# Optimization experiments

Measured on AMD Instinct MI355X. Metric: run time of the kernel, lower is better.

The kernel has to match this reference:

```python
import jax, jax.numpy as jnp
import numpy as np

CH = 512
NUM_HEADS = 8
NUM_GROUPS = 32  # min(32, channels)
EPS = 1e-5


def setup_inputs() -> dict:
    key = jax.random.key(0)
    ks = jax.random.split(key, 4)
    B, C, H, W = 8, CH, 32, 32
    x = jax.random.normal(ks[0], (B, C, H, W), dtype=jnp.float32)
    gn_weight = jnp.ones((C,), dtype=jnp.float32)
    gn_bias = jnp.zeros((C,), dtype=jnp.float32)
    # 1x1 conv weights stored as [out_ch, in_ch] (kernel dims squeezed)
    qkv_weight = jax.random.normal(ks[1], (3 * C, C), dtype=jnp.float32) * (C ** -0.5)
    qkv_bias = jnp.zeros((3 * C,), dtype=jnp.float32)
    proj_weight = jax.random.normal(ks[2], (C, C), dtype=jnp.float32) * (C ** -0.5)
    proj_bias = jnp.zeros((C,), dtype=jnp.float32)
    return {
        "x": x,
        "gn_weight": gn_weight,
        "gn_bias": gn_bias,
        "qkv_weight": qkv_weight,
        "qkv_bias": qkv_bias,
        "proj_weight": proj_weight,
        "proj_bias": proj_bias,
    }


def _group_norm(x, weight, bias):
    B, C, H, W = x.shape
    g = x.reshape(B, NUM_GROUPS, C // NUM_GROUPS, H, W)
    mean = jnp.mean(g, axis=(2, 3, 4), keepdims=True)
    var = jnp.var(g, axis=(2, 3, 4), keepdims=True)
    g = (g - mean) * jax.lax.rsqrt(var + EPS)
    g = g.reshape(B, C, H, W)
    return g * weight[None, :, None, None] + bias[None, :, None, None]


def reference(x, gn_weight, gn_bias, qkv_weight, qkv_bias, proj_weight, proj_bias):
    B, C, H, W = x.shape
    nh = NUM_HEADS
    hc = C // nh
    N = H * W

    h = _group_norm(x, gn_weight, gn_bias)
    # 1x1 conv == per-pixel matmul
    qkv = jnp.einsum('oc,bchw->bohw', qkv_weight, h) + qkv_bias[None, :, None, None]
    q, k, v = jnp.split(qkv, 3, axis=1)
    # b (h c) x y -> b h c (x y)
    q = q.reshape(B, nh, hc, N)
    k = k.reshape(B, nh, hc, N)
    v = v.reshape(B, nh, hc, N)

    scale = hc ** -0.5
    attn = jnp.einsum('bhci,bhcj->bhij', q, k) * scale  # [B, nh, N, N]
    attn = jax.nn.softmax(attn, axis=-1)
    out = jnp.einsum('bhij,bhcj->bhci', attn, v)  # [B, nh, hc, N]
    out = out.reshape(B, C, H, W)
    out = jnp.einsum('oc,bchw->bohw', proj_weight, out) + proj_bias[None, :, None, None]
    return x + out
```

## Files before the change

kernel.cpp:

```cpp
#include <hip/hip_runtime.h>
#include <math.h>

#define B_   8
#define C_   512
#define N_   1024
#define NH_  8
#define HC_  64

typedef __attribute__((ext_vector_type(8))) short bf16x8;
typedef __attribute__((ext_vector_type(4))) float f32x4;

#define MFMA16(a, b, c) __builtin_amdgcn_mfma_f32_16x16x32_bf16(a, b, c, 0, 0, 0)

__device__ __forceinline__ unsigned short f2bf(float f) {
  unsigned u = __builtin_bit_cast(unsigned, f);
  u += 0x7fffu + ((u >> 16) & 1u);
  return (unsigned short)(u >> 16);
}

__device__ __forceinline__ unsigned short f2bf_trunc(float f) {
  return (unsigned short)(__builtin_bit_cast(unsigned, f) >> 16);
}

__device__ __forceinline__ unsigned pack2(float a, float b) {
  return (unsigned)f2bf(a) | ((unsigned)f2bf(b) << 16);
}

__device__ __forceinline__ void gll16(const void* g, void* l) {
  __builtin_amdgcn_global_load_lds(
      (const __attribute__((address_space(1))) unsigned int*)g,
      (__attribute__((address_space(3))) unsigned int*)l, 16, 0, 0);
}

__global__ __launch_bounds__(256) void prep(const float* __restrict__ x,
                                            const float* __restrict__ gw,
                                            const float* __restrict__ gb,
                                            const float* __restrict__ qkvw,
                                            const float* __restrict__ pw,
                                            unsigned short* __restrict__ hT,
                                            unsigned short* __restrict__ qkvw_bf,
                                            unsigned short* __restrict__ projw_bf) {
  const int t = threadIdx.x;
  if (blockIdx.x >= 256) {
    const int widx = blockIdx.x - 256;
    const float* src = (widx < 768) ? qkvw : pw;
    unsigned short* dst = (widx < 768) ? qkvw_bf : projw_bf;
    const int i = ((widx < 768) ? widx : widx - 768) * 1024 + t * 4;
    const float4 v = *(const float4*)(src + i);
    ushort4 o;
    o.x = f2bf(v.x); o.y = f2bf(v.y); o.z = f2bf(v.z); o.w = f2bf(v.w);
    *(ushort4*)(dst + i) = o;
    return;
  }
  const int b = blockIdx.x >> 5;
  const int g = blockIdx.x & 31;
  const float* xg = x + ((size_t)b * C_ + (size_t)g * 16) * N_;

  float4 xv[16];
  float s = 0.f, ss = 0.f;
#pragma unroll
  for (int k = 0; k < 16; ++k) {
    xv[k] = *(const float4*)(xg + (size_t)k * N_ + t * 4);
    s  += xv[k].x + xv[k].y + xv[k].z + xv[k].w;
    ss += xv[k].x * xv[k].x + xv[k].y * xv[k].y + xv[k].z * xv[k].z + xv[k].w * xv[k].w;
  }
#pragma unroll
  for (int off = 32; off > 0; off >>= 1) {
    s  += __shfl_down(s, off);
    ss += __shfl_down(ss, off);
  }
  __shared__ float rs[4], rss[4], sh_mi[2];
  if ((t & 63) == 0) { rs[t >> 6] = s; rss[t >> 6] = ss; }
  __syncthreads();
  if (t == 0) {
    s  = rs[0] + rs[1] + rs[2] + rs[3];
    ss = rss[0] + rss[1] + rss[2] + rss[3];
    const float mean = s * (1.f / 16384.f);
    const float var  = ss * (1.f / 16384.f) - mean * mean;
    sh_mi[0] = mean;
    sh_mi[1] = rsqrtf(var + 1e-5f);
  }
  __syncthreads();
  const float mean = sh_mi[0], inv = sh_mi[1];

  float sc[16], of[16];
#pragma unroll
  for (int k = 0; k < 16; ++k) {
    const int c = g * 16 + k;
    sc[k] = inv * gw[c];
    of[k] = gb[c] - mean * sc[k];
  }
#pragma unroll
  for (int r = 0; r < 4; ++r) {
    const int p = t * 4 + r;
    unsigned short* dst = hT + ((size_t)b * N_ + p) * C_ + g * 16;
    uint4 o0, o1;
#pragma unroll
    for (int k2 = 0; k2 < 4; ++k2) {
      const float a0 = ((const float*)&xv[k2 * 2 + 0])[r] * sc[k2 * 2 + 0] + of[k2 * 2 + 0];
      const float a1 = ((const float*)&xv[k2 * 2 + 1])[r] * sc[k2 * 2 + 1] + of[k2 * 2 + 1];
      ((unsigned*)&o0)[k2] = pack2(a0, a1);
      const float b0 = ((const float*)&xv[8 + k2 * 2 + 0])[r] * sc[8 + k2 * 2 + 0] + of[8 + k2 * 2 + 0];
      const float b1 = ((const float*)&xv[8 + k2 * 2 + 1])[r] * sc[8 + k2 * 2 + 1] + of[8 + k2 * 2 + 1];
      ((unsigned*)&o1)[k2] = pack2(b0, b1);
    }
    *(uint4*)(dst)     = o0;
    *(uint4*)(dst + 8) = o1;
  }
}

__global__ __launch_bounds__(256, 3) void gemm_qkv(
    const unsigned short* __restrict__ A, const float* __restrict__ bias,
    const unsigned short* __restrict__ BT, unsigned short* __restrict__ qkTout,
    unsigned short* __restrict__ vout) {
  __shared__ __attribute__((aligned(16))) short lds[128 * 136];
  const int t = threadIdx.x;
  const int lane = t & 63, w = t >> 6;
  const int lm = lane & 15, q = lane >> 4;
  const int wm = w >> 1, wn = w & 1;
  const int b = blockIdx.z;
  const int m0 = blockIdx.y * 128, n0 = blockIdx.x * 128;
  const unsigned short* Bb = BT + (size_t)b * N_ * C_;

  f32x4 acc[4][4];
#pragma unroll
  for (int i = 0; i < 4; ++i)
#pragma unroll
    for (int j = 0; j < 4; ++j) acc[i][j] = (f32x4){0.f, 0.f, 0.f, 0.f};

#define QKV_STAGE(k0, base_)                                                   \
  {                                                                            \
    _Pragma("unroll") for (int rr = 0; rr < 2; ++rr) {                         \
      const int rg = w * 2 + rr;                                               \
      gll16(A  + (size_t)(m0 + rg * 16 + lm) * C_ + (k0) + q * 8,              \
            (base_) + rg * 512);                                               \
      gll16(Bb + (size_t)(n0 + rg * 16 + lm) * C_ + (k0) + q * 8,              \
            (base_) + (8 + rg) * 512);                                         \
    }                                                                          \
  }

#define QKV_COMPUTE(base_)                                                     \
  {                                                                            \
    bf16x8 af[4];                                                              \
    _Pragma("unroll") for (int mi = 0; mi < 4; ++mi)                           \
      af[mi] = *(const bf16x8*)((base_) + (wm * 4 + mi) * 512 + lane * 8);     \
    _Pragma("unroll") for (int ni = 0; ni < 4; ++ni) {                         \
      const bf16x8 bfr =                                                       \
          *(const bf16x8*)((base_) + (8 + wn * 4 + ni) * 512 + lane * 8);      \
      _Pragma("unroll") for (int mi = 0; mi < 4; ++mi)                         \
        acc[mi][ni] = MFMA16(af[mi], bfr, acc[mi][ni]);                        \
    }                                                                          \
  }

  QKV_STAGE(0, lds)
  for (int it = 0; it < 15; ++it) {
    __syncthreads();
    short* nxt = lds + ((it + 1) & 1) * 8192;
    QKV_STAGE((it + 1) * 32, nxt)
    const short* cur = lds + (it & 1) * 8192;
    QKV_COMPUTE(cur)
  }
  __syncthreads();
  QKV_COMPUTE(lds + 8192)
#undef QKV_STAGE
#undef QKV_COMPUTE

  __syncthreads();
  if (blockIdx.y < 8) {
    const float qs = (blockIdx.y < 4) ? 0.18033688011112042f : 1.0f;
#pragma unroll
    for (int mi = 0; mi < 4; ++mi) {
#pragma unroll
      for (int ni = 0; ni < 4; ++ni) {
        const int pl = wn * 64 + ni * 16 + lm;
        const int ol0 = wm * 64 + mi * 16 + q * 4;
        ushort4 o4;
        o4.x = f2bf((acc[mi][ni][0] + bias[m0 + ol0 + 0]) * qs);
        o4.y = f2bf((acc[mi][ni][1] + bias[m0 + ol0 + 1]) * qs);
        o4.z = f2bf((acc[mi][ni][2] + bias[m0 + ol0 + 2]) * qs);
        o4.w = f2bf((acc[mi][ni][3] + bias[m0 + ol0 + 3]) * qs);
        *(ushort4*)&lds[pl * 136 + ol0] = o4;
      }
    }
    __syncthreads();
#pragma unroll
    for (int u = 0; u < 8; ++u) {
      const int flat = u * 256 + t;
      const int oc = flat & 15, pl = flat >> 4;
      *(uint4*)&qkTout[((size_t)b * N_ + n0 + pl) * 1024 + m0 + oc * 8] =
          *(const uint4*)&lds[pl * 136 + oc * 8];
    }
  } else {
#pragma unroll
    for (int mi = 0; mi < 4; ++mi)
#pragma unroll
      for (int ni = 0; ni < 4; ++ni) {
        const int pl = wn * 64 + ni * 16 + lm;
#pragma unroll
        for (int r = 0; r < 4; ++r) {
          const int ol = wm * 64 + mi * 16 + q * 4 + r;
          lds[ol * 136 + pl] = f2bf(acc[mi][ni][r] + bias[m0 + ol]);
        }
      }
    __syncthreads();
    const int c0 = m0 - 1024;
#pragma unroll
    for (int u = 0; u < 8; ++u) {
      const int flat = u * 256 + t;
      const int pc = flat & 15, ol = flat >> 4;
      *(uint4*)&vout[((size_t)b * 512 + c0 + ol) * N_ + n0 + pc * 8] =
          *(const uint4*)&lds[ol * 136 + pc * 8];
    }
  }
}

__global__ __launch_bounds__(256, 4) void gemm_proj(
    const unsigned short* __restrict__ A, const float* __restrict__ bias,
    const unsigned short* __restrict__ BT, const float* __restrict__ resid,
    float* __restrict__ outf) {
  __shared__ __attribute__((aligned(16))) short lds[32 * 512];
  const int t = threadIdx.x;
  const int lane = t & 63, w = t >> 6;
  const int lm = lane & 15, q = lane >> 4;
  const int wm = w >> 1, wn = w & 1;
  const int b = blockIdx.z;
  const int m0 = blockIdx.y * 64, n0 = blockIdx.x * 64;
  const unsigned short* Bb = BT + (size_t)b * N_ * C_;

  f32x4 acc[2][2];
#pragma unroll
  for (int i = 0; i < 2; ++i)
#pragma unroll
    for (int j = 0; j < 2; ++j) acc[i][j] = (f32x4){0.f, 0.f, 0.f, 0.f};

  for (int k0 = 0; k0 < C_; k0 += 128) {
    __syncthreads();
#pragma unroll
    for (int ks = 0; ks < 4; ++ks) {
      gll16(A  + (size_t)(m0 + w * 16 + lm) * C_ + k0 + ks * 32 + q * 8,
            lds + (w * 4 + ks) * 512);
      gll16(Bb + (size_t)(n0 + w * 16 + lm) * C_ + k0 + ks * 32 + q * 8,
            lds + (16 + w * 4 + ks) * 512);
    }
    __syncthreads();
#pragma unroll
    for (int ks = 0; ks < 4; ++ks) {
      bf16x8 af[2];
#pragma unroll
      for (int mi = 0; mi < 2; ++mi)
        af[mi] = *(const bf16x8*)(lds + ((wm * 2 + mi) * 4 + ks) * 512 + lane * 8);
#pragma unroll
      for (int ni = 0; ni < 2; ++ni) {
        const bf16x8 bfr =
            *(const bf16x8*)(lds + (16 + (wn * 2 + ni) * 4 + ks) * 512 + lane * 8);
#pragma unroll
        for (int mi = 0; mi < 2; ++mi)
          acc[mi][ni] = MFMA16(af[mi], bfr, acc[mi][ni]);
      }
    }
  }

#pragma unroll
  for (int mi = 0; mi < 2; ++mi)
#pragma unroll
    for (int ni = 0; ni < 2; ++ni) {
      const int col = n0 + wn * 32 + ni * 16 + lm;
#pragma unroll
      for (int r = 0; r < 4; ++r) {
        const int row = m0 + wm * 32 + mi * 16 + q * 4 + r;
        const size_t oi = ((size_t)b * 512 + row) * N_ + col;
        outf[oi] = acc[mi][ni][r] + bias[row] + resid[oi];
      }
    }
}

__global__ __launch_bounds__(256, 6) void attn_mfma(
    const unsigned short* __restrict__ qkT, const unsigned short* __restrict__ vbuf,
    unsigned short* __restrict__ aoT) {
  __shared__ __attribute__((aligned(16))) short lds[12800];
  short* Ks = lds;
  short* Vs = lds + 8 * 512;
  short* Pb = lds + 16 * 512;

  const int t = threadIdx.x;
  const int lane = t & 63, w = t >> 6;
  const int lm = lane & 15, q = lane >> 4;
  const int id = blockIdx.x;
  const int xcd = id & 7, slot = id >> 3;
  const int pair = xcd * 8 + (slot >> 4);
  const int b = pair >> 3, hh = pair & 7;
  const int i0 = (slot & 15) * 64;

  const unsigned short* QT = qkT + (size_t)b * N_ * 1024;
  const unsigned short* Vp = vbuf + ((size_t)b * 512 + hh * 64) * N_;
  short* Pw = Pb + w * 1152;

  bf16x8 af[2];
#pragma unroll
  for (int ks = 0; ks < 2; ++ks)
    af[ks] = *(const bf16x8*)(QT + (size_t)(i0 + w * 16 + lm) * 1024 +
                              hh * 64 + ks * 32 + q * 8);

  f32x4 accO[4], lrun = (f32x4){0.f, 0.f, 0.f, 0.f};
#pragma unroll
  for (int nc = 0; nc < 4; ++nc) accO[nc] = (f32x4){0.f, 0.f, 0.f, 0.f};

  for (int jt = 0; jt < 16; ++jt) {
    const int j0 = jt * 64;
    __syncthreads();
#pragma unroll
    for (int ks = 0; ks < 2; ++ks) {
      gll16(QT + (size_t)(j0 + w * 16 + lm) * 1024 + 512 + hh * 64 + ks * 32 + q * 8,
            Ks + (w * 2 + ks) * 512);
      gll16(Vp + (size_t)(w * 16 + lm) * N_ + j0 + ks * 32 + q * 8,
            Vs + (w * 2 + ks) * 512);
    }
    __syncthreads();

    f32x4 accS[4];
#pragma unroll
    for (int nj = 0; nj < 4; ++nj) accS[nj] = (f32x4){0.f, 0.f, 0.f, 0.f};
    __builtin_amdgcn_s_setprio(1);
#pragma unroll
    for (int nj = 0; nj < 4; ++nj)
#pragma unroll
      for (int ks = 0; ks < 2; ++ks) {
        const bf16x8 bfr = *(const bf16x8*)(Ks + (nj * 2 + ks) * 512 + lane * 8);
        accS[nj] = MFMA16(af[ks], bfr, accS[nj]);
      }
    __builtin_amdgcn_s_setprio(0);

#pragma unroll
    for (int nj = 0; nj < 4; ++nj)
#pragma unroll
      for (int r = 0; r < 4; ++r) {
        const float p = __builtin_exp2f(accS[nj][r]);
        accS[nj][r] = p;
        lrun[r] += p;
      }
#pragma unroll
    for (int nj = 0; nj < 4; ++nj)
#pragma unroll
      for (int r = 0; r < 4; ++r)
        Pw[(q * 4 + r) * 72 + nj * 16 + lm] = (short)f2bf_trunc(accS[nj][r]);

    __builtin_amdgcn_s_setprio(1);
#pragma unroll
    for (int ks = 0; ks < 2; ++ks) {
      const bf16x8 pf = *(const bf16x8*)(Pw + lm * 72 + ks * 32 + q * 8);
#pragma unroll
      for (int nc = 0; nc < 4; ++nc) {
        const bf16x8 vf = *(const bf16x8*)(Vs + (nc * 2 + ks) * 512 + lane * 8);
        accO[nc] = MFMA16(pf, vf, accO[nc]);
      }
    }
    __builtin_amdgcn_s_setprio(0);
  }

#pragma unroll
  for (int d = 1; d <= 8; d <<= 1)
#pragma unroll
    for (int r = 0; r < 4; ++r) lrun[r] += __shfl_xor(lrun[r], d);
  f32x4 linv;
#pragma unroll
  for (int r = 0; r < 4; ++r) linv[r] = 1.f / lrun[r];

#pragma unroll
  for (int nc = 0; nc < 4; ++nc)
#pragma unroll
    for (int r = 0; r < 4; ++r)
      Pw[(q * 4 + r) * 72 + nc * 16 + lm] = f2bf(accO[nc][r] * linv[r]);
  unsigned short* aob = aoT + (size_t)b * N_ * C_;
#pragma unroll
  for (int u = 0; u < 2; ++u) {
    const int flat = u * 64 + lane;
    const int c8 = flat & 7, i = flat >> 3;
    *(uint4*)&aob[(size_t)(i0 + w * 16 + i) * C_ + hh * 64 + c8 * 8] =
        *(const uint4*)&Pw[i * 72 + c8 * 8];
  }
}

extern "C" void kernel_launch(void* const* d_in, const int* in_sizes, int n_in,
                              void* d_out, int out_size, void* d_ws, size_t ws_size,
                              hipStream_t stream) {
  const float* x    = (const float*)d_in[0];
  const float* gw   = (const float*)d_in[1];
  const float* gb   = (const float*)d_in[2];
  const float* qkvw = (const float*)d_in[3];
  const float* qkvb = (const float*)d_in[4];
  const float* pw   = (const float*)d_in[5];
  const float* pb   = (const float*)d_in[6];
  float* out = (float*)d_out;

  unsigned short* hT       = (unsigned short*)d_ws;
  unsigned short* qkvw_bf  = hT + (size_t)B_ * N_ * C_;
  unsigned short* projw_bf = qkvw_bf + 1536 * 512;
  unsigned short* qkT      = projw_bf + 512 * 512;
  unsigned short* vbuf     = qkT + (size_t)B_ * N_ * 1024;
  unsigned short* aoTp     = vbuf + (size_t)B_ * 512 * N_;

  prep<<<1280, 256, 0, stream>>>(x, gw, gb, qkvw, pw, hT, qkvw_bf, projw_bf);
  gemm_qkv<<<dim3(8, 12, B_), 256, 0, stream>>>(qkvw_bf, qkvb, hT, qkT, vbuf);
  attn_mfma<<<1024, 256, 0, stream>>>(qkT, vbuf, aoTp);
  gemm_proj<<<dim3(16, 8, B_), 256, 0, stream>>>(projw_bf, pb, aoTp, x, out);
}
```

Baseline: 166.4 us.

## Double-buffer LDS tiles in projection GEMM and attention K loads

The projection GEMM now uses two LDS buffers with a 64-wide k-step, so the global-to-LDS load of the next k-tile is issued before the MFMAs on the current tile run. The attention kernel double-buffers its K tiles, prefetching the next one while the current QK^T runs, and moves the wait for V to just before the PV product. The goal is to hide global-load latency behind matrix math. In exchange, attention needs more LDS and its launch bound drops from 6 to 4 blocks per CU, and the GEMM now takes twice as many barrier-separated iterations.

```diff
diff --git a/kernel.cpp b/kernel.cpp
--- a/kernel.cpp
+++ b/kernel.cpp
@@ -218,7 +218,7 @@
     const unsigned short* __restrict__ A, const float* __restrict__ bias,
     const unsigned short* __restrict__ BT, const float* __restrict__ resid,
     float* __restrict__ outf) {
-  __shared__ __attribute__((aligned(16))) short lds[32 * 512];
+  __shared__ __attribute__((aligned(16))) short lds[16384];
   const int t = threadIdx.x;
   const int lane = t & 63, w = t >> 6;
   const int lm = lane & 15, q = lane >> 4;
@@ -233,32 +233,45 @@
 #pragma unroll
     for (int j = 0; j < 2; ++j) acc[i][j] = (f32x4){0.f, 0.f, 0.f, 0.f};
 
-  for (int k0 = 0; k0 < C_; k0 += 128) {
-    __syncthreads();
-#pragma unroll
-    for (int ks = 0; ks < 4; ++ks) {
-      gll16(A  + (size_t)(m0 + w * 16 + lm) * C_ + k0 + ks * 32 + q * 8,
-            lds + (w * 4 + ks) * 512);
-      gll16(Bb + (size_t)(n0 + w * 16 + lm) * C_ + k0 + ks * 32 + q * 8,
-            lds + (16 + w * 4 + ks) * 512);
-    }
-    __syncthreads();
-#pragma unroll
-    for (int ks = 0; ks < 4; ++ks) {
-      bf16x8 af[2];
-#pragma unroll
-      for (int mi = 0; mi < 2; ++mi)
-        af[mi] = *(const bf16x8*)(lds + ((wm * 2 + mi) * 4 + ks) * 512 + lane * 8);
-#pragma unroll
-      for (int ni = 0; ni < 2; ++ni) {
-        const bf16x8 bfr =
-            *(const bf16x8*)(lds + (16 + (wn * 2 + ni) * 4 + ks) * 512 + lane * 8);
-#pragma unroll
-        for (int mi = 0; mi < 2; ++mi)
-          acc[mi][ni] = MFMA16(af[mi], bfr, acc[mi][ni]);
-      }
-    }
-  }
+#define PROJ_STAGE(k0, base_)                                                  \
+  {                                                                            \
+    _Pragma("unroll") for (int ks = 0; ks < 2; ++ks) {                         \
+      gll16(A  + (size_t)(m0 + w * 16 + lm) * C_ + (k0) + ks * 32 + q * 8,     \
+            (base_) + (w * 2 + ks) * 512);                                     \
+      gll16(Bb + (size_t)(n0 + w * 16 + lm) * C_ + (k0) + ks * 32 + q * 8,     \
+            (base_) + 4096 + (w * 2 + ks) * 512);                              \
+    }                                                                          \
+  }
+
+#define PROJ_COMPUTE(base_)                                                    \
+  {                                                                            \
+    _Pragma("unroll") for (int ks = 0; ks < 2; ++ks) {                         \
+      bf16x8 af[2];                                                            \
+      _Pragma("unroll") for (int mi = 0; mi < 2; ++mi)                         \
+        af[mi] = *(const bf16x8*)((base_) + ((wm * 2 + mi) * 2 + ks) * 512 +   \
+                                  lane * 8);                                   \
+      _Pragma("unroll") for (int ni = 0; ni < 2; ++ni) {                       \
+        const bf16x8 bfr = *(const bf16x8*)((base_) + 4096 +                   \
+                                            ((wn * 2 + ni) * 2 + ks) * 512 +   \
+                                            lane * 8);                         \
+        _Pragma("unroll") for (int mi = 0; mi < 2; ++mi)                       \
+          acc[mi][ni] = MFMA16(af[mi], bfr, acc[mi][ni]);                      \
+      }                                                                        \
+    }                                                                          \
+  }
+
+  PROJ_STAGE(0, lds)
+  for (int it = 0; it < 7; ++it) {
+    __syncthreads();
+    short* nxt = lds + ((it + 1) & 1) * 8192;
+    PROJ_STAGE((it + 1) * 64, nxt)
+    const short* cur = lds + (it & 1) * 8192;
+    PROJ_COMPUTE(cur)
+  }
+  __syncthreads();
+  PROJ_COMPUTE(lds + 8192)
+#undef PROJ_STAGE
+#undef PROJ_COMPUTE
 
 #pragma unroll
   for (int mi = 0; mi < 2; ++mi)
@@ -274,13 +287,13 @@
     }
 }
 
-__global__ __launch_bounds__(256, 6) void attn_mfma(
+__global__ __launch_bounds__(256, 4) void attn_mfma(
     const unsigned short* __restrict__ qkT, const unsigned short* __restrict__ vbuf,
     unsigned short* __restrict__ aoT) {
-  __shared__ __attribute__((aligned(16))) short lds[12800];
+  __shared__ __attribute__((aligned(16))) short lds[16896];
   short* Ks = lds;
-  short* Vs = lds + 8 * 512;
-  short* Pb = lds + 16 * 512;
+  short* Vs = lds + 8192;
+  short* Pb = lds + 12288;
 
   const int t = threadIdx.x;
   const int lane = t & 63, w = t >> 6;
@@ -305,17 +318,26 @@
 #pragma unroll
   for (int nc = 0; nc < 4; ++nc) accO[nc] = (f32x4){0.f, 0.f, 0.f, 0.f};
 
+#pragma unroll
+  for (int ks = 0; ks < 2; ++ks)
+    gll16(QT + (size_t)(w * 16 + lm) * 1024 + 512 + hh * 64 + ks * 32 + q * 8,
+          Ks + (w * 2 + ks) * 512);
+
   for (int jt = 0; jt < 16; ++jt) {
     const int j0 = jt * 64;
     __syncthreads();
 #pragma unroll
-    for (int ks = 0; ks < 2; ++ks) {
-      gll16(QT + (size_t)(j0 + w * 16 + lm) * 1024 + 512 + hh * 64 + ks * 32 + q * 8,
-            Ks + (w * 2 + ks) * 512);
+    for (int ks = 0; ks < 2; ++ks)
       gll16(Vp + (size_t)(w * 16 + lm) * N_ + j0 + ks * 32 + q * 8,
             Vs + (w * 2 + ks) * 512);
-    }
-    __syncthreads();
+    if (jt < 15) {
+#pragma unroll
+      for (int ks = 0; ks < 2; ++ks)
+        gll16(QT + (size_t)(j0 + 64 + w * 16 + lm) * 1024 + 512 + hh * 64 +
+                  ks * 32 + q * 8,
+              Ks + ((jt + 1) & 1) * 4096 + (w * 2 + ks) * 512);
+    }
+    const short* Kc = Ks + (jt & 1) * 4096;
 
     f32x4 accS[4];
 #pragma unroll
@@ -325,7 +347,7 @@
     for (int nj = 0; nj < 4; ++nj)
 #pragma unroll
       for (int ks = 0; ks < 2; ++ks) {
-        const bf16x8 bfr = *(const bf16x8*)(Ks + (nj * 2 + ks) * 512 + lane * 8);
+        const bf16x8 bfr = *(const bf16x8*)(Kc + (nj * 2 + ks) * 512 + lane * 8);
         accS[nj] = MFMA16(af[ks], bfr, accS[nj]);
       }
     __builtin_amdgcn_s_setprio(0);
@@ -343,6 +365,8 @@
 #pragma unroll
       for (int r = 0; r < 4; ++r)
         Pw[(q * 4 + r) * 72 + nj * 16 + lm] = (short)f2bf_trunc(accS[nj][r]);
+
+    __syncthreads();
 
     __builtin_amdgcn_s_setprio(1);
 #pragma unroll
```

Measured after the change: 167.7 us. Within noise of the previous version (+0.8%).

## Process two query tiles per attention block and double-buffer K loads

Applied to the files above, without the earlier changes.

Each attention block now covers 128 query rows as two 64-row tiles, so every wave reuses each K and V fragment it reads from LDS for two MFMA tiles. The grid is halved to 512 blocks and launch bounds drop to 2 blocks per CU. K tiles are double-buffered in LDS and the next tile is prefetched during the current iteration, which lets one barrier per iteration be removed. In exchange, register and LDS use per block go up and fewer waves are resident per CU, which reduces latency hiding.

```diff
diff --git a/kernel.cpp b/kernel.cpp
--- a/kernel.cpp
+++ b/kernel.cpp
@@ -274,109 +274,141 @@
     }
 }
 
-__global__ __launch_bounds__(256, 6) void attn_mfma(
+__global__ __launch_bounds__(256, 2) void attn_mfma(
     const unsigned short* __restrict__ qkT, const unsigned short* __restrict__ vbuf,
     unsigned short* __restrict__ aoT) {
-  __shared__ __attribute__((aligned(16))) short lds[12800];
+  __shared__ __attribute__((aligned(16))) short lds[21504];
   short* Ks = lds;
-  short* Vs = lds + 8 * 512;
-  short* Pb = lds + 16 * 512;
+  short* Vs = lds + 8192;
+  short* Pb = lds + 12288;
 
   const int t = threadIdx.x;
   const int lane = t & 63, w = t >> 6;
   const int lm = lane & 15, q = lane >> 4;
   const int id = blockIdx.x;
   const int xcd = id & 7, slot = id >> 3;
-  const int pair = xcd * 8 + (slot >> 4);
+  const int pair = xcd * 8 + (slot >> 3);
   const int b = pair >> 3, hh = pair & 7;
-  const int i0 = (slot & 15) * 64;
+  const int i0 = (slot & 7) * 128;
 
   const unsigned short* QT = qkT + (size_t)b * N_ * 1024;
   const unsigned short* Vp = vbuf + ((size_t)b * 512 + hh * 64) * N_;
-  short* Pw = Pb + w * 1152;
-
-  bf16x8 af[2];
+  short* Pw = Pb + w * 2304;
+
+  bf16x8 af[2][2];
+#pragma unroll
+  for (int tt = 0; tt < 2; ++tt)
+#pragma unroll
+    for (int ks = 0; ks < 2; ++ks)
+      af[tt][ks] = *(const bf16x8*)(QT +
+          (size_t)(i0 + tt * 64 + w * 16 + lm) * 1024 + hh * 64 + ks * 32 + q * 8);
+
+  f32x4 accO[2][4], lrun[2];
+#pragma unroll
+  for (int tt = 0; tt < 2; ++tt) {
+    lrun[tt] = (f32x4){0.f, 0.f, 0.f, 0.f};
+#pragma unroll
+    for (int nc = 0; nc < 4; ++nc) accO[tt][nc] = (f32x4){0.f, 0.f, 0.f, 0.f};
+  }
+
 #pragma unroll
   for (int ks = 0; ks < 2; ++ks)
-    af[ks] = *(const bf16x8*)(QT + (size_t)(i0 + w * 16 + lm) * 1024 +
-                              hh * 64 + ks * 32 + q * 8);
-
-  f32x4 accO[4], lrun = (f32x4){0.f, 0.f, 0.f, 0.f};
-#pragma unroll
-  for (int nc = 0; nc < 4; ++nc) accO[nc] = (f32x4){0.f, 0.f, 0.f, 0.f};
+    gll16(QT + (size_t)(w * 16 + lm) * 1024 + 512 + hh * 64 + ks * 32 + q * 8,
+          Ks + (w * 2 + ks) * 512);
 
   for (int jt = 0; jt < 16; ++jt) {
     const int j0 = jt * 64;
     __syncthreads();
 #pragma unroll
-    for (int ks = 0; ks < 2; ++ks) {
-      gll16(QT + (size_t)(j0 + w * 16 + lm) * 1024 + 512 + hh * 64 + ks * 32 + q * 8,
-            Ks + (w * 2 + ks) * 512);
+    for (int ks = 0; ks < 2; ++ks)
       gll16(Vp + (size_t)(w * 16 + lm) * N_ + j0 + ks * 32 + q * 8,
             Vs + (w * 2 + ks) * 512);
-    }
-    __syncthreads();
-
-    f32x4 accS[4];
-#pragma unroll
-    for (int nj = 0; nj < 4; ++nj) accS[nj] = (f32x4){0.f, 0.f, 0.f, 0.f};
+    if (jt < 15) {
+#pragma unroll
+      for (int ks = 0; ks < 2; ++ks)
+        gll16(QT + (size_t)(j0 + 64 + w * 16 + lm) * 1024 + 512 + hh * 64 +
+                  ks * 32 + q * 8,
+              Ks + ((jt + 1) & 1) * 4096 + (w * 2 + ks) * 512);
+    }
+    const short* Kc = Ks + (jt & 1) * 4096;
+
+    f32x4 accS[2][4];
+#pragma unroll
+    for (int tt = 0; tt < 2; ++tt)
+#pragma unroll
+      for (int nj = 0; nj < 4; ++nj) accS[tt][nj] = (f32x4){0.f, 0.f, 0.f, 0.f};
     __builtin_amdgcn_s_setprio(1);
 #pragma unroll
     for (int nj = 0; nj < 4; ++nj)
 #pragma unroll
       for (int ks = 0; ks < 2; ++ks) {
-        const bf16x8 bfr = *(const bf16x8*)(Ks + (nj * 2 + ks) * 512 + lane * 8);
-        accS[nj] = MFMA16(af[ks], bfr, accS[nj]);
+        const bf16x8 bfr = *(const bf16x8*)(Kc + (nj * 2 + ks) * 512 + lane * 8);
+        accS[0][nj] = MFMA16(af[0][ks], bfr, accS[0][nj]);
+        accS[1][nj] = MFMA16(af[1][ks], bfr, accS[1][nj]);
       }
     __builtin_amdgcn_s_setprio(0);
 
 #pragma unroll
-    for (int nj = 0; nj < 4; ++nj)
-#pragma unroll
-      for (int r = 0; r < 4; ++r) {
-        const float p = __builtin_exp2f(accS[nj][r]);
-        accS[nj][r] = p;
-        lrun[r] += p;
-      }
-#pragma unroll
-    for (int nj = 0; nj < 4; ++nj)
-#pragma unroll
-      for (int r = 0; r < 4; ++r)
-        Pw[(q * 4 + r) * 72 + nj * 16 + lm] = (short)f2bf_trunc(accS[nj][r]);
+    for (int tt = 0; tt < 2; ++tt)
+#pragma unroll
+      for (int nj = 0; nj < 4; ++nj)
+#pragma unroll
+        for (int r = 0; r < 4; ++r) {
+          const float p = __builtin_exp2f(accS[tt][nj][r]);
+          accS[tt][nj][r] = p;
+          lrun[tt][r] += p;
+        }
+#pragma unroll
+    for (int tt = 0; tt < 2; ++tt)
+#pragma unroll
+      for (int nj = 0; nj < 4; ++nj)
+#pragma unroll
+        for (int r = 0; r < 4; ++r)
+          Pw[tt * 1152 + (q * 4 + r) * 72 + nj * 16 + lm] =
+              (short)f2bf_trunc(accS[tt][nj][r]);
+
+    __syncthreads();
 
     __builtin_amdgcn_s_setprio(1);
 #pragma unroll
     for (int ks = 0; ks < 2; ++ks) {
-      const bf16x8 pf = *(const bf16x8*)(Pw + lm * 72 + ks * 32 + q * 8);
+      const bf16x8 pf0 = *(const bf16x8*)(Pw + lm * 72 + ks * 32 + q * 8);
+      const bf16x8 pf1 = *(const bf16x8*)(Pw + 1152 + lm * 72 + ks * 32 + q * 8);
 #pragma unroll
       for (int nc = 0; nc < 4; ++nc) {
         const bf16x8 vf = *(const bf16x8*)(Vs + (nc * 2 + ks) * 512 + lane * 8);
-        accO[nc] = MFMA16(pf, vf, accO[nc]);
+        accO[0][nc] = MFMA16(pf0, vf, accO[0][nc]);
+        accO[1][nc] = MFMA16(pf1, vf, accO[1][nc]);
       }
     }
     __builtin_amdgcn_s_setprio(0);
   }
 
-#pragma unroll
-  for (int d = 1; d <= 8; d <<= 1)
-#pragma unroll
-    for (int r = 0; r < 4; ++r) lrun[r] += __shfl_xor(lrun[r], d);
-  f32x4 linv;
-#pragma unroll
-  for (int r = 0; r < 4; ++r) linv[r] = 1.f / lrun[r];
-
-#pragma unroll
-  for (int nc = 0; nc < 4; ++nc)
-#pragma unroll
-    for (int r = 0; r < 4; ++r)
-      Pw[(q * 4 + r) * 72 + nc * 16 + lm] = f2bf(accO[nc][r] * linv[r]);
   unsigned short* aob = aoT + (size_t)b * N_ * C_;
 #pragma unroll
-  for (int u = 0; u < 2; ++u) {
-    const int flat = u * 64 + lane;
-    const int c8 = flat & 7, i = flat >> 3;
-    *(uint4*)&aob[(size_t)(i0 + w * 16 + i) * C_ + hh * 64 + c8 * 8] =
-        *(const uint4*)&Pw[i * 72 + c8 * 8];
+  for (int tt = 0; tt < 2; ++tt) {
+    f32x4 lr = lrun[tt];
+#pragma unroll
+    for (int d = 1; d <= 8; d <<= 1)
+#pragma unroll
+      for (int r = 0; r < 4; ++r) lr[r] += __shfl_xor(lr[r], d);
+    f32x4 linv;
+#pragma unroll
+    for (int r = 0; r < 4; ++r) linv[r] = 1.f / lr[r];
+
+#pragma unroll
+    for (int nc = 0; nc < 4; ++nc)
+#pragma unroll
+      for (int r = 0; r < 4; ++r)
+        Pw[tt * 1152 + (q * 4 + r) * 72 + nc * 16 + lm] =
+            f2bf(accO[tt][nc][r] * linv[r]);
+#pragma unroll
+    for (int u = 0; u < 2; ++u) {
+      const int flat = u * 64 + lane;
+      const int c8 = flat & 7, i = flat >> 3;
+      *(uint4*)&aob[(size_t)(i0 + tt * 64 + w * 16 + i) * C_ + hh * 64 + c8 * 8] =
+          *(const uint4*)&Pw[tt * 1152 + i * 72 + c8 * 8];
+    }
   }
 }
 
@@ -401,6 +433,6 @@
 
   prep<<<1280, 256, 0, stream>>>(x, gw, gb, qkvw, pw, hT, qkvw_bf, projw_bf);
   gemm_qkv<<<dim3(8, 12, B_), 256, 0, stream>>>(qkvw_bf, qkvb, hT, qkT, vbuf);
-  attn_mfma<<<1024, 256, 0, stream>>>(qkT, vbuf, aoTp);
+  attn_mfma<<<512, 256, 0, stream>>>(qkT, vbuf, aoTp);
   gemm_proj<<<dim3(16, 8, B_), 256, 0, stream>>>(projw_bf, pb, aoTp, x, out);
 }
```

Result: no change. 165.9 us (-0.3%).

## Rework attention kernel around 32x32 MFMA with 128-row query tiles and K double-buffering

Applied to the files above, without the earlier changes.

The attention kernel now uses 32x32x16 bf16 MFMAs, with each block covering 128 query rows (32 per wave) instead of 64. The grid shrinks to 512 blocks. K tiles are double-buffered so the next tile's load overlaps current compute, and the P tile is written to LDS in an XOR-swizzled layout to avoid bank conflicts. The softmax row sum is computed with an MFMA against a ones vector instead of per-lane adds and shuffles. In exchange, occupancy drops (launch bounds go from 6 to 2 blocks per CU, with more LDS and registers), and an extra barrier is added per iteration.

```diff
diff --git a/kernel.cpp b/kernel.cpp
--- a/kernel.cpp
+++ b/kernel.cpp
@@ -9,8 +9,10 @@
 
 typedef __attribute__((ext_vector_type(8))) short bf16x8;
 typedef __attribute__((ext_vector_type(4))) float f32x4;
+typedef __attribute__((ext_vector_type(16))) float f32x16;
 
 #define MFMA16(a, b, c) __builtin_amdgcn_mfma_f32_16x16x32_bf16(a, b, c, 0, 0, 0)
+#define MFMA32(a, b, c) __builtin_amdgcn_mfma_f32_32x32x16_bf16(a, b, c, 0, 0, 0)
 
 __device__ __forceinline__ unsigned short f2bf(float f) {
   unsigned u = __builtin_bit_cast(unsigned, f);
@@ -274,109 +276,137 @@
     }
 }
 
-__global__ __launch_bounds__(256, 6) void attn_mfma(
+__global__ __launch_bounds__(256, 2) void attn_mfma(
     const unsigned short* __restrict__ qkT, const unsigned short* __restrict__ vbuf,
     unsigned short* __restrict__ aoT) {
-  __shared__ __attribute__((aligned(16))) short lds[12800];
+  __shared__ __attribute__((aligned(16))) short lds[21504];
   short* Ks = lds;
-  short* Vs = lds + 8 * 512;
-  short* Pb = lds + 16 * 512;
+  short* Vs = lds + 8192;
+  short* Pb = lds + 12288;
 
   const int t = threadIdx.x;
-  const int lane = t & 63, w = t >> 6;
-  const int lm = lane & 15, q = lane >> 4;
+  const int l = t & 63, w = t >> 6;
+  const int l31 = l & 31, lh = l >> 5;
   const int id = blockIdx.x;
   const int xcd = id & 7, slot = id >> 3;
-  const int pair = xcd * 8 + (slot >> 4);
+  const int pair = xcd * 8 + (slot >> 3);
   const int b = pair >> 3, hh = pair & 7;
-  const int i0 = (slot & 15) * 64;
+  const int i0 = (slot & 7) * 128;
 
   const unsigned short* QT = qkT + (size_t)b * N_ * 1024;
   const unsigned short* Vp = vbuf + ((size_t)b * 512 + hh * 64) * N_;
-  short* Pw = Pb + w * 1152;
-
-  bf16x8 af[2];
-#pragma unroll
-  for (int ks = 0; ks < 2; ++ks)
-    af[ks] = *(const bf16x8*)(QT + (size_t)(i0 + w * 16 + lm) * 1024 +
-                              hh * 64 + ks * 32 + q * 8);
-
-  f32x4 accO[4], lrun = (f32x4){0.f, 0.f, 0.f, 0.f};
-#pragma unroll
-  for (int nc = 0; nc < 4; ++nc) accO[nc] = (f32x4){0.f, 0.f, 0.f, 0.f};
+  short* Pw = Pb + w * 2304;
+  char* Pwb = (char*)Pw;
+
+  bf16x8 af[4];
+#pragma unroll
+  for (int kc = 0; kc < 4; ++kc)
+    af[kc] = *(const bf16x8*)(QT + (size_t)(i0 + w * 32 + l31) * 1024 +
+                              hh * 64 + kc * 16 + lh * 8);
+
+  bf16x8 ones;
+#pragma unroll
+  for (int e = 0; e < 8; ++e) ones[e] = (short)0x3F80;
+
+  f32x16 accO[2], accL;
+#pragma unroll
+  for (int r2 = 0; r2 < 16; ++r2) {
+    accL[r2] = 0.f; accO[0][r2] = 0.f; accO[1][r2] = 0.f;
+  }
+
+#pragma unroll
+  for (int rr = 0; rr < 2; ++rr) {
+    const int idx = w * 2 + rr, jb = idx >> 2, kc = idx & 3;
+    gll16(QT + (size_t)(jb * 32 + l31) * 1024 + 512 + hh * 64 + kc * 16 + lh * 8,
+          Ks + idx * 512);
+  }
+
+  const int e2 = (l & 7) << 1;
+  const int keyb = ((l31 >> 3) & 1) << 6;
+  const int wbase0 = (((l31 >> 3) & 1) << 9) + (lh << 6) + e2;
+  const int prd = ((l >> 3) & 7) << 4;
 
   for (int jt = 0; jt < 16; ++jt) {
     const int j0 = jt * 64;
     __syncthreads();
 #pragma unroll
-    for (int ks = 0; ks < 2; ++ks) {
-      gll16(QT + (size_t)(j0 + w * 16 + lm) * 1024 + 512 + hh * 64 + ks * 32 + q * 8,
-            Ks + (w * 2 + ks) * 512);
-      gll16(Vp + (size_t)(w * 16 + lm) * N_ + j0 + ks * 32 + q * 8,
-            Vs + (w * 2 + ks) * 512);
-    }
-    __syncthreads();
-
-    f32x4 accS[4];
-#pragma unroll
-    for (int nj = 0; nj < 4; ++nj) accS[nj] = (f32x4){0.f, 0.f, 0.f, 0.f};
+    for (int rr = 0; rr < 2; ++rr) {
+      const int idx = w * 2 + rr, nc = idx >> 2, kj = idx & 3;
+      gll16(Vp + (size_t)(nc * 32 + l31) * N_ + j0 + kj * 16 + lh * 8,
+            Vs + idx * 512);
+    }
+    if (jt < 15) {
+#pragma unroll
+      for (int rr = 0; rr < 2; ++rr) {
+        const int idx = w * 2 + rr, jb = idx >> 2, kc = idx & 3;
+        gll16(QT + (size_t)(j0 + 64 + jb * 32 + l31) * 1024 + 512 + hh * 64 +
+                  kc * 16 + lh * 8,
+              Ks + ((jt + 1) & 1) * 4096 + idx * 512);
+      }
+    }
+    const short* Kc = Ks + (jt & 1) * 4096;
+
+    f32x16 accS[2];
+#pragma unroll
+    for (int r2 = 0; r2 < 16; ++r2) { accS[0][r2] = 0.f; accS[1][r2] = 0.f; }
     __builtin_amdgcn_s_setprio(1);
 #pragma unroll
-    for (int nj = 0; nj < 4; ++nj)
-#pragma unroll
-      for (int ks = 0; ks < 2; ++ks) {
-        const bf16x8 bfr = *(const bf16x8*)(Ks + (nj * 2 + ks) * 512 + lane * 8);
-        accS[nj] = MFMA16(af[ks], bfr, accS[nj]);
+    for (int kc = 0; kc < 4; ++kc)
+#pragma unroll
+      for (int jb = 0; jb < 2; ++jb) {
+        const bf16x8 bfr = *(const bf16x8*)(Kc + (jb * 4 + kc) * 512 + l * 8);
+        accS[jb] = MFMA32(af[kc], bfr, accS[jb]);
       }
     __builtin_amdgcn_s_setprio(0);
 
 #pragma unroll
-    for (int nj = 0; nj < 4; ++nj)
-#pragma unroll
-      for (int r = 0; r < 4; ++r) {
-        const float p = __builtin_exp2f(accS[nj][r]);
-        accS[nj][r] = p;
-        lrun[r] += p;
-      }
-#pragma unroll
-    for (int nj = 0; nj < 4; ++nj)
-#pragma unroll
-      for (int r = 0; r < 4; ++r)
-        Pw[(q * 4 + r) * 72 + nj * 16 + lm] = (short)f2bf_trunc(accS[nj][r]);
+    for (int jb = 0; jb < 2; ++jb) {
+      const int base = ((jb * 2 + (l31 >> 4)) << 10) + wbase0;
+#pragma unroll
+      for (int rg = 0; rg < 16; ++rg) {
+        const float p = __builtin_exp2f(accS[jb][rg]);
+        const int byte = (base + ((rg & 3) << 4) + ((rg >> 2) << 7)) ^
+                         ((((rg >> 2) << 4)) | keyb);
+        *(short*)(Pwb + byte) = (short)f2bf_trunc(p);
+      }
+    }
+
+    __syncthreads();
 
     __builtin_amdgcn_s_setprio(1);
-#pragma unroll
-    for (int ks = 0; ks < 2; ++ks) {
-      const bf16x8 pf = *(const bf16x8*)(Pw + lm * 72 + ks * 32 + q * 8);
-#pragma unroll
-      for (int nc = 0; nc < 4; ++nc) {
-        const bf16x8 vf = *(const bf16x8*)(Vs + (nc * 2 + ks) * 512 + lane * 8);
-        accO[nc] = MFMA16(pf, vf, accO[nc]);
-      }
-    }
+    bf16x8 pa[4];
+#pragma unroll
+    for (int kj = 0; kj < 4; ++kj)
+      pa[kj] = *(const bf16x8*)(Pwb + ((kj << 10) + ((l * 16) ^ prd)));
+#pragma unroll
+    for (int nc = 0; nc < 2; ++nc)
+#pragma unroll
+      for (int kj = 0; kj < 4; ++kj) {
+        const bf16x8 vf = *(const bf16x8*)(Vs + (nc * 4 + kj) * 512 + l * 8);
+        accO[nc] = MFMA32(pa[kj], vf, accO[nc]);
+      }
+#pragma unroll
+    for (int kj = 0; kj < 4; ++kj) accL = MFMA32(pa[kj], ones, accL);
     __builtin_amdgcn_s_setprio(0);
   }
 
-#pragma unroll
-  for (int d = 1; d <= 8; d <<= 1)
-#pragma unroll
-    for (int r = 0; r < 4; ++r) lrun[r] += __shfl_xor(lrun[r], d);
-  f32x4 linv;
-#pragma unroll
-  for (int r = 0; r < 4; ++r) linv[r] = 1.f / lrun[r];
-
-#pragma unroll
-  for (int nc = 0; nc < 4; ++nc)
-#pragma unroll
-    for (int r = 0; r < 4; ++r)
-      Pw[(q * 4 + r) * 72 + nc * 16 + lm] = f2bf(accO[nc][r] * linv[r]);
+  float linv[16];
+#pragma unroll
+  for (int rg = 0; rg < 16; ++rg) linv[rg] = 1.f / accL[rg];
+#pragma unroll
+  for (int nc = 0; nc < 2; ++nc)
+#pragma unroll
+    for (int rg = 0; rg < 16; ++rg) {
+      const int rowi = (rg & 3) + ((rg >> 2) << 3) + (lh << 2);
+      Pw[rowi * 72 + nc * 32 + l31] = (short)f2bf(accO[nc][rg] * linv[rg]);
+    }
   unsigned short* aob = aoT + (size_t)b * N_ * C_;
 #pragma unroll
-  for (int u = 0; u < 2; ++u) {
-    const int flat = u * 64 + lane;
-    const int c8 = flat & 7, i = flat >> 3;
-    *(uint4*)&aob[(size_t)(i0 + w * 16 + i) * C_ + hh * 64 + c8 * 8] =
-        *(const uint4*)&Pw[i * 72 + c8 * 8];
+  for (int u = 0; u < 4; ++u) {
+    const int flat = u * 64 + l;
+    const int c8 = flat & 7, row = flat >> 3;
+    *(uint4*)&aob[(size_t)(i0 + w * 32 + row) * C_ + hh * 64 + c8 * 8] =
+        *(const uint4*)&Pw[row * 72 + c8 * 8];
   }
 }
 
@@ -401,6 +431,6 @@
 
   prep<<<1280, 256, 0, stream>>>(x, gw, gb, qkvw, pw, hT, qkvw_bf, projw_bf);
   gemm_qkv<<<dim3(8, 12, B_), 256, 0, stream>>>(qkvw_bf, qkvb, hT, qkT, vbuf);
-  attn_mfma<<<1024, 256, 0, stream>>>(qkT, vbuf, aoTp);
+  attn_mfma<<<512, 256, 0, stream>>>(qkT, vbuf, aoTp);
   gemm_proj<<<dim3(16, 8, B_), 256, 0, stream>>>(projw_bf, pb, aoTp, x, out);
 }
```

New measurement: 162.3 us. 2.5% less time.
